# Kernel optimization log

Measured on AMD Instinct MI355X. Metric: run time of the kernel, lower is better.

## Reference

```python
import jax, jax.numpy as jnp
import numpy as np

HEADS = 8
DIM_HEAD = 64
EPS = 1e-5


def _layernorm(x, g, b):
    m = jnp.mean(x, axis=-1, keepdims=True)
    v = jnp.mean((x - m) ** 2, axis=-1, keepdims=True)
    return (x - m) * jax.lax.rsqrt(v + EPS) * g + b


def setup_inputs() -> dict:
    key = jax.random.key(0)
    ks = jax.random.split(key, 8)
    b, c, hh, ww = 4, 256, 48, 48
    inner = HEADS * DIM_HEAD  # 512
    s = 0.02
    return {
        "x": jax.random.normal(ks[0], (b, c, hh, ww), jnp.float32),
        "Wq": jax.random.normal(ks[1], (c, inner), jnp.float32) * s,
        "Wk": jax.random.normal(ks[2], (c, inner), jnp.float32) * s,
        "Wv": jax.random.normal(ks[3], (c, inner), jnp.float32) * s,
        "Wo": jax.random.normal(ks[4], (inner, c), jnp.float32) * s,
        "bo": jnp.zeros((c,), jnp.float32),
        "g1": jnp.ones((c,), jnp.float32),
        "b1": jnp.zeros((c,), jnp.float32),
        "g2": jnp.ones((c,), jnp.float32),
        "b2": jnp.zeros((c,), jnp.float32),
        "Wf1": jax.random.normal(ks[5], (c, 2 * c), jnp.float32) * s,
        "bf1": jnp.zeros((2 * c,), jnp.float32),
        "Wf2": jax.random.normal(ks[6], (2 * c, c), jnp.float32) * s,
        "bf2": jnp.zeros((c,), jnp.float32),
        "Wp": jax.random.normal(ks[7], (c, c), jnp.float32) * s,
        "bp": jnp.zeros((c,), jnp.float32),
    }


def reference(x, Wq, Wk, Wv, Wo, bo, g1, b1, g2, b2, Wf1, bf1, Wf2, bf2, Wp, bp):
    b, c, hh, ww = x.shape
    n = hh * ww
    scale = DIM_HEAD ** -0.5
    x_in = x
    t = jnp.transpose(x.reshape(b, c, n), (0, 2, 1))  # [b, n, c]

    # --- CrossAttention (self-attn, context=None) ---
    tn = _layernorm(t, g1, b1)
    q = (tn @ Wq).reshape(b, n, HEADS, DIM_HEAD)
    k = (tn @ Wk).reshape(b, n, HEADS, DIM_HEAD)
    v = (tn @ Wv).reshape(b, n, HEADS, DIM_HEAD)
    sim = jnp.einsum("bihd,bjhd->bhij", q, k) * scale  # [b,h,n,n]
    attn = jax.nn.softmax(sim, axis=-1)
    o = jnp.einsum("bhij,bjhd->bihd", attn, v).reshape(b, n, HEADS * DIM_HEAD)
    t = o @ Wo + bo + t

    # --- FeedForward: Linear -> GELU(exact) -> Linear ---
    f = jax.nn.gelu(_layernorm(t, g2, b2) @ Wf1 + bf1, approximate=False)
    t = f @ Wf2 + bf2 + t

    # back to image and 1x1 conv (Wp[c_in, c_out])
    xi = jnp.transpose(t, (0, 2, 1)).reshape(b, c, hh, ww)
    y = jnp.einsum("bchw,co->bohw", xi, Wp) + bp[None, :, None, None]
    return y + x_in
```

## Files before the change

### kernel.cpp

```cpp
#include <hip/hip_runtime.h>
#include <math.h>

#define B_    4
#define C_    256
#define N_    2304
#define H_    8
#define DH_   64
#define IN_   512
#define ROWS_ 9216
#define NHALF 576

typedef __attribute__((ext_vector_type(8))) short short8;
typedef __attribute__((ext_vector_type(4))) float f32x4;
typedef __attribute__((ext_vector_type(16))) float f32x16;

__device__ __forceinline__ unsigned short f2bf(float f) {
    unsigned int u = __float_as_uint(f);
    u += 0x7fffu + ((u >> 16) & 1u);
    return (unsigned short)(u >> 16);
}

__device__ __forceinline__ float bf2f(unsigned short u) {
    return __uint_as_float(((unsigned)u) << 16);
}

__device__ __forceinline__ float fexp2(float x) {
    return __builtin_amdgcn_exp2f(x);
}

__device__ __forceinline__ float gelu_fast(float x) {
    float x2 = x * x;
    float u  = x * fmaf(0.044715f, x2, 1.0f);
    float e  = fexp2(-2.3022082f * u);
    return x * __builtin_amdgcn_rcpf(1.0f + e);
}

__device__ __forceinline__ unsigned cvtpk(float lo, float hi) {
    unsigned r;
    asm("v_cvt_pk_bf16_f32 %0, %1, %2" : "=v"(r) : "v"(lo), "v"(hi));
    return r;
}

__device__ __forceinline__ void gload_lds16(const void* g, void* l) {
    __builtin_amdgcn_global_load_lds(
        (const __attribute__((address_space(1))) unsigned int*)g,
        (__attribute__((address_space(3))) unsigned int*)l, 16, 0, 0);
}

__device__ __forceinline__ const short8* frg(const short* base, int row, int chunk) {
    return (const short8*)(base + (row << 6) + (((chunk) ^ (row & 7)) << 3));
}

__device__ __forceinline__ int swz2(int row) {
    return (row & 7) ^ ((row >> 3) & 3);
}
__device__ __forceinline__ const short8* frg2(const short* base, int row, int chunk) {
    return (const short8*)(base + (row << 6) + (((chunk) ^ swz2(row)) << 3));
}

__global__ __launch_bounds__(256)
void k_pre(const float* __restrict__ Wq, const float* __restrict__ Wk,
           const float* __restrict__ Wv, const float* __restrict__ Wo,
           const float* __restrict__ Wf1, const float* __restrict__ Wf2,
           const float* __restrict__ Wp,
           unsigned short* Wqh, unsigned short* Wkh, unsigned short* Wvh,
           unsigned short* Woh, unsigned short* Wf1h, unsigned short* Wf2h,
           unsigned short* Wph,
           const float* __restrict__ x, float* __restrict__ T,
           unsigned short* __restrict__ TNh,
           const float* __restrict__ g1, const float* __restrict__ b1) {
    __shared__ float tile[32][257];
    int bid = blockIdx.x;
    int tid = threadIdx.x;
    if (bid < 1792) {
        int wz = bid >> 8;
        int rem = bid & 255;
        int nBase = (rem & 15) * 32;
        int kBase = (rem >> 4) * 32;
        const float* src; unsigned short* dst; int K, N;
        switch (wz) {
            case 0: src = Wq;  dst = Wqh;  K = 256; N = 512; break;
            case 1: src = Wk;  dst = Wkh;  K = 256; N = 512; break;
            case 2: src = Wv;  dst = Wvh;  K = 256; N = 512; break;
            case 3: src = Wo;  dst = Woh;  K = 512; N = 256; break;
            case 4: src = Wf1; dst = Wf1h; K = 256; N = 512; break;
            case 5: src = Wf2; dst = Wf2h; K = 512; N = 256; break;
            default: src = Wp; dst = Wph;  K = 256; N = 256; break;
        }
        if (nBase >= N || kBase >= K) return;
        float scl = (wz == 0) ? 0.18033688f : 1.0f;
        int tx = tid & 31, ty = tid >> 5;
        #pragma unroll
        for (int i = 0; i < 32; i += 8)
            tile[ty + i][tx] = src[(size_t)(kBase + ty + i) * N + nBase + tx];
        __syncthreads();
        #pragma unroll
        for (int i = 0; i < 32; i += 8)
            dst[(size_t)(nBase + ty + i) * K + kBase + tx] = f2bf(tile[tx][ty + i] * scl);
    } else {
        int idx = bid - 1792;
        int bb = idx / 72;
        int nBase = (idx - bb * 72) * 32;
        int tx = tid & 31;
        int tg = tid >> 5;
        const float* xp = x + (size_t)bb * C_ * N_ + nBase + tx;
        #pragma unroll
        for (int i = 0; i < 32; ++i) {
            int c = tg * 32 + i;
            tile[tx][c] = xp[(size_t)c * N_];
        }
        __syncthreads();
        int w = tid >> 6, lane = tid & 63;
        float g0 = g1[lane], ga = g1[lane + 64], gb2 = g1[lane + 128], gc = g1[lane + 192];
        float b0 = b1[lane], ba = b1[lane + 64], bb2 = b1[lane + 128], bc = b1[lane + 192];
        #pragma unroll
        for (int r8 = 0; r8 < 8; ++r8) {
            int row = w * 8 + r8;
            float v0 = tile[row][lane],       v1 = tile[row][lane + 64];
            float v2 = tile[row][lane + 128], v3 = tile[row][lane + 192];
            float s = v0 + v1 + v2 + v3;
            #pragma unroll
            for (int m = 1; m < 64; m <<= 1) s += __shfl_xor(s, m);
            float mean = s * (1.0f / C_);
            float d0 = v0 - mean, d1 = v1 - mean, d2 = v2 - mean, d3 = v3 - mean;
            float s2 = d0 * d0 + d1 * d1 + d2 * d2 + d3 * d3;
            #pragma unroll
            for (int m = 1; m < 64; m <<= 1) s2 += __shfl_xor(s2, m);
            float rs = rsqrtf(s2 * (1.0f / C_) + 1e-5f);
            size_t o = (size_t)(bb * N_ + nBase + row) * C_ + lane;
            T[o]       = v0; T[o + 64]  = v1; T[o + 128] = v2; T[o + 192] = v3;
            TNh[o]       = f2bf(d0 * rs * g0 + b0);
            TNh[o + 64]  = f2bf(d1 * rs * ga + ba);
            TNh[o + 128] = f2bf(d2 * rs * gb2 + bb2);
            TNh[o + 192] = f2bf(d3 * rs * gc + bc);
        }
    }
}

__global__ __launch_bounds__(256)
void k_layernorm_bf16(const float* __restrict__ in, unsigned short* __restrict__ out,
                      const float* __restrict__ g, const float* __restrict__ b) {
    int wv = threadIdx.x >> 6;
    int lane = threadIdx.x & 63;
    int row = blockIdx.x * 4 + wv;
    float4 v = ((const float4*)(in + (size_t)row * C_))[lane];
    float s = v.x + v.y + v.z + v.w;
    #pragma unroll
    for (int m = 1; m < 64; m <<= 1) s += __shfl_xor(s, m);
    float mean = s * (1.0f / C_);
    float dx = v.x - mean, dy = v.y - mean, dz = v.z - mean, dw = v.w - mean;
    float s2 = dx * dx + dy * dy + dz * dz + dw * dw;
    #pragma unroll
    for (int m = 1; m < 64; m <<= 1) s2 += __shfl_xor(s2, m);
    float rs = rsqrtf(s2 * (1.0f / C_) + 1e-5f);
    float4 gv = ((const float4*)g)[lane];
    float4 bv = ((const float4*)b)[lane];
    ushort4 o;
    o.x = f2bf(dx * rs * gv.x + bv.x);
    o.y = f2bf(dy * rs * gv.y + bv.y);
    o.z = f2bf(dz * rs * gv.z + bv.z);
    o.w = f2bf(dw * rs * gv.w + bv.w);
    *(ushort4*)(out + (size_t)row * C_ + lane * 4) = o;
}

template <int EP>
__global__ __launch_bounds__(256)
void k_gemm64(const short* __restrict__ A, const short* __restrict__ Bt,
              void* __restrict__ Out, const float* __restrict__ bias,
              const float* __restrict__ Res, int M, int N, int K) {
    __shared__ __align__(16) short As[64 * 64];
    __shared__ __align__(16) short Bs[64 * 64];
    int tid = threadIdx.x;
    int w = tid >> 6;
    int lane = tid & 63;
    int l15 = lane & 15;
    int lg = lane >> 4;
    int wr = w >> 1, wc = w & 1;
    int rowBase = blockIdx.y * 64;
    int colBase = blockIdx.x * 64;

    f32x4 acc[2][2];
    #pragma unroll
    for (int m = 0; m < 2; ++m)
        #pragma unroll
        for (int n = 0; n < 2; ++n) acc[m][n] = (f32x4){0.f, 0.f, 0.f, 0.f};

    for (int k0 = 0; k0 < K; k0 += 64) {
        __syncthreads();
        #pragma unroll
        for (int a = 0; a < 2; ++a) {
            int rr = (w << 4) + (a << 3) + (lane >> 3);
            int cc = (lane & 7) ^ (lane >> 3);
            gload_lds16(A + (size_t)(rowBase + rr) * K + k0 + cc * 8,
                        As + (((w << 4) + (a << 3)) << 6));
            gload_lds16(Bt + (size_t)(colBase + rr) * K + k0 + cc * 8,
                        Bs + (((w << 4) + (a << 3)) << 6));
        }
        asm volatile("s_waitcnt vmcnt(0)" ::: "memory");
        __syncthreads();
        short8 af[2][2], bf[2][2];
        #pragma unroll
        for (int m = 0; m < 2; ++m) {
            af[m][0] = *frg(As, wr * 32 + m * 16 + l15, lg);
            af[m][1] = *frg(As, wr * 32 + m * 16 + l15, 4 + lg);
        }
        #pragma unroll
        for (int n = 0; n < 2; ++n) {
            bf[n][0] = *frg(Bs, wc * 32 + n * 16 + l15, lg);
            bf[n][1] = *frg(Bs, wc * 32 + n * 16 + l15, 4 + lg);
        }
        #pragma unroll
        for (int m = 0; m < 2; ++m)
            #pragma unroll
            for (int n = 0; n < 2; ++n) {
                acc[m][n] = __builtin_amdgcn_mfma_f32_16x16x32_bf16(af[m][0], bf[n][0], acc[m][n], 0, 0, 0);
                acc[m][n] = __builtin_amdgcn_mfma_f32_16x16x32_bf16(af[m][1], bf[n][1], acc[m][n], 0, 0, 0);
            }
    }

    int arB = rowBase + wr * 32;
    int brB = colBase + wc * 32;
    int bb = 0;
    if (EP == 5) bb = brB / N_;
    #pragma unroll
    for (int m = 0; m < 2; ++m) {
        #pragma unroll
        for (int i = 0; i < 4; ++i) {
            int ar = arB + m * 16 + lg * 4 + i;
            #pragma unroll
            for (int n = 0; n < 2; ++n) {
                int br = brB + n * 16 + l15;
                float v = acc[m][n][i];
                if constexpr (EP == 2) {
                    size_t o = (size_t)ar * N + br;
                    ((float*)Out)[o] = v + bias[br] + Res[o];
                } else if constexpr (EP == 3) {
                    ((unsigned short*)Out)[(size_t)ar * N + br] = f2bf(gelu_fast(v + bias[br]));
                } else if constexpr (EP == 4) {
                    size_t o = (size_t)ar * N + br;
                    ((unsigned short*)Out)[o] = f2bf(v + bias[br] + Res[o]);
                } else {
                    size_t o = ((size_t)(bb * C_) + ar) * N_ + (br - bb * N_);
                    ((float*)Out)[o] = v + bias[ar] + Res[o];
                }
            }
        }
    }
}

__global__ __launch_bounds__(256)
void k_gemm_qkv(const short* __restrict__ TNh, const short* __restrict__ Wqh,
                const short* __restrict__ Wkh, const short* __restrict__ Wvh,
                unsigned short* __restrict__ Qb, unsigned short* __restrict__ Kb,
                unsigned short* __restrict__ Vt) {
    __shared__ __align__(16) short As[64 * 64];
    __shared__ __align__(16) short Bs[64 * 64];
    int bid = blockIdx.x;
    int z = bid / 1152;
    int rem = bid - z * 1152;
    int tid = threadIdx.x;
    int w = tid >> 6;
    int lane = tid & 63;
    int l15 = lane & 15;
    int lg = lane >> 4;
    int wr = w >> 1, wc = w & 1;
    const short *A, *Bt;
    int rowBase, colBase;
    if (z < 2) {
        A = TNh; Bt = z ? Wkh : Wqh;
        colBase = (rem & 7) * 64;
        rowBase = (rem >> 3) * 64;
    } else {
        A = Wvh; Bt = TNh;
        colBase = (rem % 144) * 64;
        rowBase = (rem / 144) * 64;
    }
    const int K = C_;

    f32x4 acc[2][2];
    #pragma unroll
    for (int m = 0; m < 2; ++m)
        #pragma unroll
        for (int n = 0; n < 2; ++n) acc[m][n] = (f32x4){0.f, 0.f, 0.f, 0.f};

    for (int k0 = 0; k0 < K; k0 += 64) {
        __syncthreads();
        #pragma unroll
        for (int a = 0; a < 2; ++a) {
            int rr = (w << 4) + (a << 3) + (lane >> 3);
            int cc = (lane & 7) ^ (lane >> 3);
            gload_lds16(A + (size_t)(rowBase + rr) * K + k0 + cc * 8,
                        As + (((w << 4) + (a << 3)) << 6));
            gload_lds16(Bt + (size_t)(colBase + rr) * K + k0 + cc * 8,
                        Bs + (((w << 4) + (a << 3)) << 6));
        }
        asm volatile("s_waitcnt vmcnt(0)" ::: "memory");
        __syncthreads();
        short8 af[2][2], bf[2][2];
        #pragma unroll
        for (int m = 0; m < 2; ++m) {
            af[m][0] = *frg(As, wr * 32 + m * 16 + l15, lg);
            af[m][1] = *frg(As, wr * 32 + m * 16 + l15, 4 + lg);
        }
        #pragma unroll
        for (int n = 0; n < 2; ++n) {
            bf[n][0] = *frg(Bs, wc * 32 + n * 16 + l15, lg);
            bf[n][1] = *frg(Bs, wc * 32 + n * 16 + l15, 4 + lg);
        }
        #pragma unroll
        for (int m = 0; m < 2; ++m)
            #pragma unroll
            for (int n = 0; n < 2; ++n) {
                acc[m][n] = __builtin_amdgcn_mfma_f32_16x16x32_bf16(af[m][0], bf[n][0], acc[m][n], 0, 0, 0);
                acc[m][n] = __builtin_amdgcn_mfma_f32_16x16x32_bf16(af[m][1], bf[n][1], acc[m][n], 0, 0, 0);
            }
    }

    int arB = rowBase + wr * 32;
    int brB = colBase + wc * 32;
    if (z < 2) {
        unsigned short* Out = z ? Kb : Qb;
        #pragma unroll
        for (int m = 0; m < 2; ++m)
            #pragma unroll
            for (int i = 0; i < 4; ++i) {
                int ar = arB + m * 16 + lg * 4 + i;
                #pragma unroll
                for (int n = 0; n < 2; ++n)
                    Out[(size_t)ar * IN_ + brB + n * 16 + l15] = f2bf(acc[m][n][i]);
            }
    } else {
        int bb = brB / N_;
        #pragma unroll
        for (int m = 0; m < 2; ++m)
            #pragma unroll
            for (int i = 0; i < 4; ++i) {
                int ar = arB + m * 16 + lg * 4 + i;
                #pragma unroll
                for (int n = 0; n < 2; ++n) {
                    int br = brB + n * 16 + l15;
                    Vt[((size_t)(bb * IN_) + ar) * N_ + (br - bb * N_)] = f2bf(acc[m][n][i]);
                }
            }
    }
}

__global__ __launch_bounds__(256, 3)
void k_flash_mfma(const short* __restrict__ Qb, const short* __restrict__ Kb,
                  const short* __restrict__ Vt,
                  unsigned short* O0, unsigned short* O1,
                  unsigned short* O2, unsigned short* O3,
                  float* __restrict__ Lsum) {
    __shared__ __align__(16) short Ks[2][64 * 64];
    __shared__ __align__(16) short Vs[2][64 * 64];
    int tid = threadIdx.x;
    int lane = tid & 63;
    int l31 = lane & 31;
    int h5 = lane >> 5;
    int w = tid >> 6;

    int logical = (blockIdx.x & 7) * 288 + (blockIdx.x >> 3);
    int pair = logical / 18;
    int qi = logical - pair * 18;
    int bh = pair & 31;
    int half = pair >> 5;
    int bb = bh >> 3, h = bh & 7;
    int qBase = qi * 128;
    int h0 = half * NHALF;

    const short* Qp = Qb + ((size_t)bb * N_ + qBase + w * 32) * IN_ + h * DH_;
    const short* Kp = Kb + (size_t)bb * N_ * IN_ + h * DH_;
    const short* Vp = Vt + ((size_t)bb * IN_ + h * DH_) * N_;

    short8 qf[4];
    #pragma unroll
    for (int kk = 0; kk < 4; ++kk)
        qf[kk] = *(const short8*)(Qp + (size_t)l31 * IN_ + kk * 16 + h5 * 8);

    short8 ones;
    #pragma unroll
    for (int j = 0; j < 8; ++j) ones[j] = (short)0x3F80;

    auto STAGE = [&](int buf, int kt2) {
        #pragma unroll
        for (int j = 0; j < 2; ++j) {
            int br = (w << 4) + (j << 3);
            int rr = br + (lane >> 3);
            int cc = (lane & 7) ^ (lane >> 3) ^ ((2 * w + j) & 3);
            gload_lds16(Kp + (size_t)(kt2 + rr) * IN_ + cc * 8, &Ks[buf][br << 6]);
            gload_lds16(Vp + (size_t)rr * N_ + kt2 + cc * 8, &Vs[buf][br << 6]);
        }
    };

    f32x16 oacc0 = (f32x16)(0.0f);
    f32x16 oacc1 = (f32x16)(0.0f);
    f32x16 lacc  = (f32x16)(0.0f);

    STAGE(0, h0);
    const int NT = NHALF / 64;
    for (int t = 0; t < NT; ++t) {
        asm volatile("s_waitcnt vmcnt(0)" ::: "memory");
        __builtin_amdgcn_s_barrier();
        __builtin_amdgcn_sched_barrier(0);
        if (t + 1 < NT) STAGE((t + 1) & 1, h0 + (t + 1) * 64);
        const short* Kc = Ks[t & 1];
        const short* Vc = Vs[t & 1];

        short8 pa[4];
        #pragma unroll
        for (int s = 0; s < 2; ++s) {
            f32x16 stv = (f32x16)(0.0f);
            __builtin_amdgcn_s_setprio(1);
            #pragma unroll
            for (int kk = 0; kk < 4; ++kk) {
                short8 kf = *frg2(Kc, s * 32 + l31, kk * 2 + h5);
                stv = __builtin_amdgcn_mfma_f32_32x32x16_bf16(kf, qf[kk], stv, 0, 0, 0);
            }
            __builtin_amdgcn_s_setprio(0);
            unsigned u[8];
            #pragma unroll
            for (int q = 0; q < 4; ++q) {
                u[2 * q]     = cvtpk(fexp2(stv[4 * q + 0]), fexp2(stv[4 * q + 1]));
                u[2 * q + 1] = cvtpk(fexp2(stv[4 * q + 2]), fexp2(stv[4 * q + 3]));
            }
            asm volatile("v_permlane32_swap_b32 %0, %1" : "+v"(u[0]), "+v"(u[2]));
            asm volatile("v_permlane32_swap_b32 %0, %1" : "+v"(u[1]), "+v"(u[3]));
            asm volatile("v_permlane32_swap_b32 %0, %1" : "+v"(u[4]), "+v"(u[6]));
            asm volatile("v_permlane32_swap_b32 %0, %1" : "+v"(u[5]), "+v"(u[7]));
            union { unsigned uu[4]; short8 s8; } c0, c1;
            c0.uu[0] = u[0]; c0.uu[1] = u[1]; c0.uu[2] = u[2]; c0.uu[3] = u[3];
            c1.uu[0] = u[4]; c1.uu[1] = u[5]; c1.uu[2] = u[6]; c1.uu[3] = u[7];
            pa[2 * s]     = c0.s8;
            pa[2 * s + 1] = c1.s8;
        }

        __builtin_amdgcn_s_setprio(1);
        #pragma unroll
        for (int kk = 0; kk < 4; ++kk) {
            short8 vf0 = *frg2(Vc, l31, kk * 2 + h5);
            short8 vf1 = *frg2(Vc, 32 + l31, kk * 2 + h5);
            lacc  = __builtin_amdgcn_mfma_f32_32x32x16_bf16(pa[kk], ones, lacc, 0, 0, 0);
            oacc0 = __builtin_amdgcn_mfma_f32_32x32x16_bf16(pa[kk], vf0, oacc0, 0, 0, 0);
            oacc1 = __builtin_amdgcn_mfma_f32_32x32x16_bf16(pa[kk], vf1, oacc1, 0, 0, 0);
        }
        __builtin_amdgcn_s_setprio(0);
    }

    unsigned short* OpH = (half == 0) ? O0 : (half == 1) ? O1 : (half == 2) ? O2 : O3;
    unsigned short* Op = OpH + ((size_t)bb * N_ + qBase + w * 32) * IN_ + h * DH_;
    #pragma unroll
    for (int reg = 0; reg < 16; ++reg) {
        int q = (reg & 3) + 8 * (reg >> 2) + 4 * h5;
        Op[(size_t)q * IN_ + l31]      = f2bf(oacc0[reg]);
        Op[(size_t)q * IN_ + 32 + l31] = f2bf(oacc1[reg]);
    }
    if (l31 == 0) {
        float* Lp = Lsum + (((size_t)half * B_ + bb) * H_ + h) * N_ + qBase + w * 32;
        #pragma unroll
        for (int reg = 0; reg < 16; ++reg) {
            int q = (reg & 3) + 8 * (reg >> 2) + 4 * h5;
            Lp[q] = lacc[reg];
        }
    }
}

__global__ __launch_bounds__(256)
void k_combine(const unsigned short* p0, const unsigned short* p1,
               const unsigned short* p2, const unsigned short* p3,
               const float* __restrict__ Lsum, unsigned short* Ob) {
    int wv = threadIdx.x >> 6;
    int lane = threadIdx.x & 63;
    int row = blockIdx.x * 4 + wv;
    int bb = row / N_;
    int n = row - bb * N_;
    int hh = lane >> 3;
    float l = 0.f;
    #pragma unroll
    for (int q4 = 0; q4 < 4; ++q4)
        l += Lsum[(((size_t)q4 * B_ + bb) * H_ + hh) * N_ + n];
    float inv = 1.0f / l;
    size_t off = (size_t)row * IN_ + lane * 8;
    short8 a0 = *(const short8*)(p0 + off);
    short8 a1 = *(const short8*)(p1 + off);
    short8 a2 = *(const short8*)(p2 + off);
    short8 a3 = *(const short8*)(p3 + off);
    unsigned short o[8];
    #pragma unroll
    for (int j = 0; j < 8; ++j)
        o[j] = f2bf((bf2f((unsigned short)a0[j]) + bf2f((unsigned short)a1[j]) +
                     bf2f((unsigned short)a2[j]) + bf2f((unsigned short)a3[j])) * inv);
    *(uint4*)(Ob + off) = *(uint4*)o;
}

extern "C" void kernel_launch(void* const* d_in, const int* in_sizes, int n_in,
                              void* d_out, int out_size, void* d_ws, size_t ws_size,
                              hipStream_t stream) {
    (void)in_sizes; (void)n_in; (void)out_size; (void)ws_size;
    const float* x   = (const float*)d_in[0];
    const float* Wq  = (const float*)d_in[1];
    const float* Wk  = (const float*)d_in[2];
    const float* Wv  = (const float*)d_in[3];
    const float* Wo  = (const float*)d_in[4];
    const float* bo  = (const float*)d_in[5];
    const float* g1  = (const float*)d_in[6];
    const float* b1  = (const float*)d_in[7];
    const float* g2  = (const float*)d_in[8];
    const float* b2  = (const float*)d_in[9];
    const float* Wf1 = (const float*)d_in[10];
    const float* bf1 = (const float*)d_in[11];
    const float* Wf2 = (const float*)d_in[12];
    const float* bf2 = (const float*)d_in[13];
    const float* Wp  = (const float*)d_in[14];
    const float* bp  = (const float*)d_in[15];
    float* out = (float*)d_out;
    float* ws  = (float*)d_ws;

    float* T    = ws;
    float* T2   = ws + 2359296;
    unsigned short* TNh = (unsigned short*)(ws + 4718592);
    short* Qb   = (short*)(ws + 5898240);
    short* Kb   = (short*)(ws + 8257536);
    short* Vt   = (short*)(ws + 10616832);
    unsigned short* Obh = (unsigned short*)(ws + 12976128);
    short* F    = (short*)(ws + 15335424);
    short* T3h  = (short*)(ws + 17694720);
    unsigned short* Wqh  = (unsigned short*)(ws + 18874368);
    unsigned short* Wkh  = (unsigned short*)(ws + 18939904);
    unsigned short* Wvh  = (unsigned short*)(ws + 19005440);
    unsigned short* Woh  = (unsigned short*)(ws + 19070976);
    unsigned short* Wf1h = (unsigned short*)(ws + 19136512);
    unsigned short* Wf2h = (unsigned short*)(ws + 19202048);
    unsigned short* Wph  = (unsigned short*)(ws + 19267584);
    unsigned short* Op0  = (unsigned short*)(ws + 19398656);
    unsigned short* Op3  = (unsigned short*)(ws + 21757952);
    unsigned short* Op1  = Obh;
    unsigned short* Op2  = (unsigned short*)F;
    float* Lsum = ws + 24117248;

    k_pre<<<dim3(2080), 256, 0, stream>>>(Wq, Wk, Wv, Wo, Wf1, Wf2, Wp,
                                          Wqh, Wkh, Wvh, Woh, Wf1h, Wf2h, Wph,
                                          x, T, TNh, g1, b1);
    k_gemm_qkv<<<dim3(3456), 256, 0, stream>>>((const short*)TNh, (const short*)Wqh,
                                               (const short*)Wkh, (const short*)Wvh,
                                               (unsigned short*)Qb, (unsigned short*)Kb,
                                               (unsigned short*)Vt);
    k_flash_mfma<<<dim3(2304), 256, 0, stream>>>(Qb, Kb, Vt, Op0, Op1, Op2, Op3, Lsum);
    k_combine<<<2304, 256, 0, stream>>>(Op0, Op1, Op2, Op3, Lsum, Obh);
    k_gemm64<2><<<dim3(4, 144), 256, 0, stream>>>((const short*)Obh, (const short*)Woh, T2, bo, T, ROWS_, C_, IN_);
    k_layernorm_bf16<<<2304, 256, 0, stream>>>(T2, TNh, g2, b2);
    k_gemm64<3><<<dim3(8, 144), 256, 0, stream>>>((const short*)TNh, (const short*)Wf1h, F, bf1, nullptr, ROWS_, IN_, C_);
    k_gemm64<4><<<dim3(4, 144), 256, 0, stream>>>((const short*)F, (const short*)Wf2h, T3h, bf2, T2, ROWS_, C_, IN_);
    k_gemm64<5><<<dim3(144, 4), 256, 0, stream>>>((const short*)Wph, (const short*)T3h, out, bp, x, C_, ROWS_, C_);
}
```

Baseline: 142.1 us.

## Double-buffer LDS tiles in GEMM kernels to overlap loads with MFMA

Both bf16 GEMM kernels get two LDS buffers per operand. The next K-tile's global-to-LDS load is issued right after the barrier, before the current tile's MFMAs, and one of the two barriers per iteration is dropped. The goal is to hide global load latency behind compute. In exchange, LDS use per block doubles, which may cut occupancy. With K of 256 or 512 there are only 4-8 iterations, so the pipeline is short.

```diff
diff --git a/kernel.cpp b/kernel.cpp
--- a/kernel.cpp
+++ b/kernel.cpp
@@ -168,8 +168,8 @@
 void k_gemm64(const short* __restrict__ A, const short* __restrict__ Bt,
               void* __restrict__ Out, const float* __restrict__ bias,
               const float* __restrict__ Res, int M, int N, int K) {
-    __shared__ __align__(16) short As[64 * 64];
-    __shared__ __align__(16) short Bs[64 * 64];
+    __shared__ __align__(16) short As[2][64 * 64];
+    __shared__ __align__(16) short Bs[2][64 * 64];
     int tid = threadIdx.x;
     int w = tid >> 6;
     int lane = tid & 63;
@@ -179,35 +179,44 @@
     int rowBase = blockIdx.y * 64;
     int colBase = blockIdx.x * 64;
 
-    f32x4 acc[2][2];
-    #pragma unroll
-    for (int m = 0; m < 2; ++m)
-        #pragma unroll
-        for (int n = 0; n < 2; ++n) acc[m][n] = (f32x4){0.f, 0.f, 0.f, 0.f};
-
-    for (int k0 = 0; k0 < K; k0 += 64) {
-        __syncthreads();
+    auto STAGE = [&](int buf, int k0) {
         #pragma unroll
         for (int a = 0; a < 2; ++a) {
-            int rr = (w << 4) + (a << 3) + (lane >> 3);
+            int br = (w << 4) + (a << 3);
+            int rr = br + (lane >> 3);
             int cc = (lane & 7) ^ (lane >> 3);
             gload_lds16(A + (size_t)(rowBase + rr) * K + k0 + cc * 8,
-                        As + (((w << 4) + (a << 3)) << 6));
+                        &As[buf][br << 6]);
             gload_lds16(Bt + (size_t)(colBase + rr) * K + k0 + cc * 8,
-                        Bs + (((w << 4) + (a << 3)) << 6));
-        }
+                        &Bs[buf][br << 6]);
+        }
+    };
+
+    f32x4 acc[2][2];
+    #pragma unroll
+    for (int m = 0; m < 2; ++m)
+        #pragma unroll
+        for (int n = 0; n < 2; ++n) acc[m][n] = (f32x4){0.f, 0.f, 0.f, 0.f};
+
+    STAGE(0, 0);
+    int NK = K >> 6;
+    for (int t = 0; t < NK; ++t) {
         asm volatile("s_waitcnt vmcnt(0)" ::: "memory");
-        __syncthreads();
+        __builtin_amdgcn_s_barrier();
+        __builtin_amdgcn_sched_barrier(0);
+        if (t + 1 < NK) STAGE((t + 1) & 1, (t + 1) << 6);
+        const short* Ac = As[t & 1];
+        const short* Bc = Bs[t & 1];
         short8 af[2][2], bf[2][2];
         #pragma unroll
         for (int m = 0; m < 2; ++m) {
-            af[m][0] = *frg(As, wr * 32 + m * 16 + l15, lg);
-            af[m][1] = *frg(As, wr * 32 + m * 16 + l15, 4 + lg);
+            af[m][0] = *frg(Ac, wr * 32 + m * 16 + l15, lg);
+            af[m][1] = *frg(Ac, wr * 32 + m * 16 + l15, 4 + lg);
         }
         #pragma unroll
         for (int n = 0; n < 2; ++n) {
-            bf[n][0] = *frg(Bs, wc * 32 + n * 16 + l15, lg);
-            bf[n][1] = *frg(Bs, wc * 32 + n * 16 + l15, 4 + lg);
+            bf[n][0] = *frg(Bc, wc * 32 + n * 16 + l15, lg);
+            bf[n][1] = *frg(Bc, wc * 32 + n * 16 + l15, 4 + lg);
         }
         #pragma unroll
         for (int m = 0; m < 2; ++m)
@@ -253,8 +262,8 @@
                 const short* __restrict__ Wkh, const short* __restrict__ Wvh,
                 unsigned short* __restrict__ Qb, unsigned short* __restrict__ Kb,
                 unsigned short* __restrict__ Vt) {
-    __shared__ __align__(16) short As[64 * 64];
-    __shared__ __align__(16) short Bs[64 * 64];
+    __shared__ __align__(16) short As[2][64 * 64];
+    __shared__ __align__(16) short Bs[2][64 * 64];
     int bid = blockIdx.x;
     int z = bid / 1152;
     int rem = bid - z * 1152;
@@ -277,35 +286,44 @@
     }
     const int K = C_;
 
-    f32x4 acc[2][2];
-    #pragma unroll
-    for (int m = 0; m < 2; ++m)
-        #pragma unroll
-        for (int n = 0; n < 2; ++n) acc[m][n] = (f32x4){0.f, 0.f, 0.f, 0.f};
-
-    for (int k0 = 0; k0 < K; k0 += 64) {
-        __syncthreads();
+    auto STAGE = [&](int buf, int k0) {
         #pragma unroll
         for (int a = 0; a < 2; ++a) {
-            int rr = (w << 4) + (a << 3) + (lane >> 3);
+            int br = (w << 4) + (a << 3);
+            int rr = br + (lane >> 3);
             int cc = (lane & 7) ^ (lane >> 3);
             gload_lds16(A + (size_t)(rowBase + rr) * K + k0 + cc * 8,
-                        As + (((w << 4) + (a << 3)) << 6));
+                        &As[buf][br << 6]);
             gload_lds16(Bt + (size_t)(colBase + rr) * K + k0 + cc * 8,
-                        Bs + (((w << 4) + (a << 3)) << 6));
-        }
+                        &Bs[buf][br << 6]);
+        }
+    };
+
+    f32x4 acc[2][2];
+    #pragma unroll
+    for (int m = 0; m < 2; ++m)
+        #pragma unroll
+        for (int n = 0; n < 2; ++n) acc[m][n] = (f32x4){0.f, 0.f, 0.f, 0.f};
+
+    STAGE(0, 0);
+    const int NK = K >> 6;
+    for (int t = 0; t < NK; ++t) {
         asm volatile("s_waitcnt vmcnt(0)" ::: "memory");
-        __syncthreads();
+        __builtin_amdgcn_s_barrier();
+        __builtin_amdgcn_sched_barrier(0);
+        if (t + 1 < NK) STAGE((t + 1) & 1, (t + 1) << 6);
+        const short* Ac = As[t & 1];
+        const short* Bc = Bs[t & 1];
         short8 af[2][2], bf[2][2];
         #pragma unroll
         for (int m = 0; m < 2; ++m) {
-            af[m][0] = *frg(As, wr * 32 + m * 16 + l15, lg);
-            af[m][1] = *frg(As, wr * 32 + m * 16 + l15, 4 + lg);
+            af[m][0] = *frg(Ac, wr * 32 + m * 16 + l15, lg);
+            af[m][1] = *frg(Ac, wr * 32 + m * 16 + l15, 4 + lg);
         }
         #pragma unroll
         for (int n = 0; n < 2; ++n) {
-            bf[n][0] = *frg(Bs, wc * 32 + n * 16 + l15, lg);
-            bf[n][1] = *frg(Bs, wc * 32 + n * 16 + l15, 4 + lg);
+            bf[n][0] = *frg(Bc, wc * 32 + n * 16 + l15, lg);
+            bf[n][1] = *frg(Bc, wc * 32 + n * 16 + l15, 4 + lg);
         }
         #pragma unroll
         for (int m = 0; m < 2; ++m)
```

After: 146.1 us. 1.03x slower.
